# Kernel tuning notes

Hardware: AMD Instinct MI355X
Metric: run time of the kernel (lower is better)

Reference implementation:

```python
import jax, jax.numpy as jnp
import numpy as np

K = 20
NEG = jnp.float32(-1e30)

def _l2norm(x):
    # F.normalize(x, dim=1, p=2) with eps clamp
    n = jnp.sqrt(jnp.sum(x * x, axis=1, keepdims=True))
    return x / jnp.maximum(n, 1e-12)

def setup_inputs() -> dict:
    key = jax.random.key(0)
    k1, k2, k3 = jax.random.split(key, 3)
    h, w, C = 96, 96, 256
    query_label = jax.random.randint(k1, (h, w, 3), 0, 2, dtype=jnp.int64)
    color = jnp.zeros((3,), dtype=jnp.int64)
    q_feat = jax.random.normal(k2, (1, C, h, w), dtype=jnp.float32)
    s_feat = jax.random.normal(k3, (1, C, h, w), dtype=jnp.float32)
    return {"query_label": query_label, "color": color, "q_feat": q_feat, "s_feat": s_feat}

def reference(query_label, color, q_feat, s_feat):
    C = q_feat.shape[1]
    out_hw = s_feat.shape[2:]
    # mask at feature resolution (query_label already sized [h,w,3])
    mask = jnp.all(query_label == color, axis=-1).reshape(-1)      # [M]
    q = q_feat[0].transpose(1, 2, 0).reshape(-1, C)                # [M,C]
    s = s_feat[0].transpose(1, 2, 0).reshape(-1, C)                # [N,C]
    qn = _l2norm(q)
    sn = _l2norm(s)
    sim = sn @ qn.T                                                # [N,M] cosine sims
    # top-K over fg columns == top-K over full row with non-fg masked to -inf
    fg_top = jax.lax.top_k(jnp.where(mask[None, :], sim, NEG), K)[0]
    bg_top = jax.lax.top_k(jnp.where(mask[None, :], NEG, sim), K)[0]
    fg_score = jnp.mean(fg_top, axis=1).reshape(out_hw)
    bg_score = jnp.mean(bg_top, axis=1).reshape(out_hw)
    return fg_score, bg_score
```

## Files before the change

### kernel.cpp

```cpp
#include <hip/hip_runtime.h>
#include <math.h>

#define MTOT 9216
#define CDIM 256
#define KSEL 20
#define NCHUNK 4
#define CHUNKQ 2304
#define BS 32
#define QSTEP 128
#define NSTEP 18
#define NSLAB 72

typedef __attribute__((ext_vector_type(8))) short short8;
typedef __attribute__((ext_vector_type(8))) unsigned short ushort8;
typedef __attribute__((ext_vector_type(4))) float f32x4;
typedef __attribute__((ext_vector_type(2))) _Float16 h2;

__device__ __forceinline__ unsigned short f2bf(float v) {
    unsigned u = __float_as_uint(v);
    u += 0x7FFF + ((u >> 16) & 1);
    return (unsigned short)(u >> 16);
}
__device__ __forceinline__ h2 pkh2(float lo, float hi) {
    auto r = __builtin_amdgcn_cvt_pkrtz(lo, hi);
    h2 h; __builtin_memcpy(&h, &r, 4); return h;
}
__device__ __forceinline__ h2 asH2(unsigned int u) {
    h2 h; __builtin_memcpy(&h, &u, 4); return h;
}
__device__ __forceinline__ unsigned int h2u(h2 h) {
    unsigned int u; __builtin_memcpy(&u, &h, 4); return u;
}
__device__ __forceinline__ h2 h2max(h2 a, h2 b) { return __builtin_elementwise_max(a, b); }
__device__ __forceinline__ h2 h2min(h2 a, h2 b) { return __builtin_elementwise_min(a, b); }
__device__ __forceinline__ unsigned short hbits(_Float16 x) {
    unsigned short u; __builtin_memcpy(&u, &x, 2); return u;
}
__device__ __forceinline__ float hs2f(unsigned short u) {
    _Float16 x; __builtin_memcpy(&x, &u, 2); return (float)x;
}

__device__ __forceinline__ void ins20p(h2 (&l)[KSEL], h2 v) {
    v = h2max(v, l[0]);
#pragma unroll
    for (int i = 0; i < KSEL - 1; ++i) {
        h2 nxt = l[i + 1];
        l[i] = h2min(nxt, v);
        v = h2max(nxt, v);
    }
    l[KSEL - 1] = v;
}
__device__ __forceinline__ void ins20(float (&l)[KSEL], float v) {
#pragma unroll
    for (int i = 0; i < KSEL - 1; ++i) {
        float nxt = l[i + 1];
        l[i] = fminf(nxt, v);
        v = fmaxf(nxt, v);
    }
    l[KSEL - 1] = v;
}

__global__ __launch_bounds__(256) void prepconv_kernel(
    const int* __restrict__ ql, const int* __restrict__ color,
    const float* __restrict__ qf, const float* __restrict__ sf,
    int* __restrict__ cnt,
    unsigned short* __restrict__ qbt, unsigned short* __restrict__ sbt)
{
    __shared__ float tilef[32 * 257];
    __shared__ float red[256];
    __shared__ float invv[32];
    __shared__ int slotl[32];
    const int bid = blockIdx.x;
    const bool isQ = bid < (MTOT / 32);
    const int m0 = (isQ ? bid : bid - MTOT / 32) * 32;
    const float* src = isQ ? qf : sf;
    const int t = threadIdx.x;
    const int ml = t & 31, cb = t >> 5;
    float sq = 0.f;
#pragma unroll
    for (int i = 0; i < 32; ++i) {
        int c = cb * 32 + i;
        float v = src[c * MTOT + m0 + ml];
        tilef[ml * 257 + c] = v;
        sq += v * v;
    }
    red[cb * 32 + ml] = sq;
    __syncthreads();
    if (t < 32) {
        float s = 0.f;
#pragma unroll
        for (int j = 0; j < 8; ++j) s += red[j * 32 + t];
        invv[t] = 1.0f / fmaxf(sqrtf(s), 1e-12f);
        if (isQ) {
            int m = m0 + t;
            bool fg = (ql[3*m] == color[0]) & (ql[3*m+1] == color[1]) & (ql[3*m+2] == color[2]);
            slotl[t] = fg ? atomicAdd(&cnt[0], 1) : (MTOT - 1 - atomicAdd(&cnt[1], 1));
        }
    }
    __syncthreads();
    const int row = t >> 3, seg = t & 7;
    const float iv = invv[row];
    const int drow = isQ ? slotl[row] : (m0 + row);
    unsigned short* dst = (isQ ? qbt : sbt) + (size_t)drow * 256 + seg * 32;
    const float* srcr = &tilef[row * 257 + seg * 32];
#pragma unroll
    for (int ch = 0; ch < 4; ++ch) {
        ushort8 o;
#pragma unroll
        for (int e = 0; e < 8; ++e) o[e] = f2bf(srcr[ch * 8 + e] * iv);
        *(ushort8*)(dst + ch * 8) = o;
    }
}

__global__ __launch_bounds__(256, 3) void matchsim_kernel(
    const unsigned short* __restrict__ qbt, const unsigned short* __restrict__ sbt,
    const int* __restrict__ cnt, unsigned short* __restrict__ part)
{
    __shared__ __align__(16) char smem[49152];
    unsigned int* mbuf = (unsigned int*)smem;

    const int t = threadIdx.x;
    const int w = t >> 6, l = t & 63;
    const int sblk = blockIdx.x >> 2;
    const int chunk = blockIdx.x & 3;
    const int s0 = sblk * BS;
    const int q0c = chunk * CHUNKQ;
    const int fgc = cnt[0];

    {
        int row = t >> 3, cb = t & 7;
        const ushort8* gs = (const ushort8*)(sbt + (size_t)(s0 + row) * 256);
#pragma unroll
        for (int i = 0; i < 4; ++i) {
            int ch = cb + i * 8;
            ushort8 v = gs[ch];
            int byte = (row * 512 + ch * 16) ^ ((row & 7) << 4);
            *(ushort8*)(smem + byte) = v;
        }
    }

    const h2 NEG2 = { (_Float16)-65504.f, (_Float16)-65504.f };
    h2 fgl[KSEL], bgl[KSEL];
#pragma unroll
    for (int i = 0; i < KSEL; ++i) { fgl[i] = NEG2; bgl[i] = NEG2; }

    ushort8 qr[4];
    const int qrow_w = t >> 1, qhalf = t & 1;
    auto loadQ = [&](int gslab) {
        int step = gslab >> 2, slab = gslab & 3;
        const unsigned short* base =
            qbt + (size_t)(q0c + step * QSTEP + qrow_w) * 256 + slab * 64 + qhalf * 32;
#pragma unroll
        for (int i = 0; i < 4; ++i)
            qr[i] = *(const ushort8*)(base + i * 8);
    };
    loadQ(0);
    const int qwswz = (qrow_w & 7) << 4;

    const int lg = l >> 4;
    const int aq0 = w * 32 + (l & 15);
    const int aq1 = aq0 + 16;
    const int aswz0 = (aq0 & 7) << 4, aswz1 = (aq1 & 7) << 4;
    const int srow0 = l & 15, srow1 = srow0 + 16;
    const int bswz0 = (srow0 & 7) << 4, bswz1 = (srow1 & 7) << 4;

    f32x4 acc00 = {0,0,0,0}, acc01 = {0,0,0,0}, acc10 = {0,0,0,0}, acc11 = {0,0,0,0};
    int cur = 0;

    for (int gslab = 0; gslab < NSLAB; ++gslab) {
        char* Qs = smem + 16384 + cur * 16384;
#pragma unroll
        for (int i = 0; i < 4; ++i) {
            int byte = (qrow_w * 128 + qhalf * 64 + i * 16) ^ qwswz;
            *(ushort8*)(Qs + byte) = qr[i];
        }
        if (gslab + 1 < NSLAB) loadQ(gslab + 1);
        __syncthreads();
        const int slab = gslab & 3;
#pragma unroll
        for (int ks = 0; ks < 2; ++ks) {
            int ak = ks * 64 + lg * 16;
            short8 a0 = *(const short8*)(Qs + ((aq0 * 128 + ak) ^ aswz0));
            short8 a1 = *(const short8*)(Qs + ((aq1 * 128 + ak) ^ aswz1));
            int bk = slab * 128 + ks * 64 + lg * 16;
            short8 b0 = *(const short8*)(smem + ((srow0 * 512 + bk) ^ bswz0));
            short8 b1 = *(const short8*)(smem + ((srow1 * 512 + bk) ^ bswz1));
            acc00 = __builtin_amdgcn_mfma_f32_16x16x32_bf16(a0, b0, acc00, 0, 0, 0);
            acc01 = __builtin_amdgcn_mfma_f32_16x16x32_bf16(a0, b1, acc01, 0, 0, 0);
            acc10 = __builtin_amdgcn_mfma_f32_16x16x32_bf16(a1, b0, acc10, 0, 0, 0);
            acc11 = __builtin_amdgcn_mfma_f32_16x16x32_bf16(a1, b1, acc11, 0, 0, 0);
        }
        cur ^= 1;
        if (slab == 3) {
            const int step = gslab >> 2;
            const int qw0 = q0c + step * QSTEP + w * 32;
#pragma unroll
            for (int qt = 0; qt < 2; ++qt) {
                const f32x4& aS0 = qt ? acc10 : acc00;
                const f32x4& aS1 = qt ? acc11 : acc01;
                int qfirst = qw0 + qt * 16;
                if (qfirst + 16 <= fgc) {
#pragma unroll
                    for (int r = 0; r < 4; ++r) ins20p(fgl, pkh2(aS0[r], aS1[r]));
                } else if (qfirst >= fgc) {
#pragma unroll
                    for (int r = 0; r < 4; ++r) ins20p(bgl, pkh2(aS0[r], aS1[r]));
                } else {
#pragma unroll
                    for (int r = 0; r < 4; ++r) {
                        h2 v = pkh2(aS0[r], aS1[r]);
                        bool m = (qfirst + lg * 4 + r) < fgc;
                        ins20p(fgl, m ? v : NEG2);
                        ins20p(bgl, m ? NEG2 : v);
                    }
                }
            }
            acc00 = (f32x4){0,0,0,0}; acc01 = (f32x4){0,0,0,0};
            acc10 = (f32x4){0,0,0,0}; acc11 = (f32x4){0,0,0,0};
        }
    }

    __syncthreads();
    const int sp = l & 15, owner = w * 4 + lg;
    auto midx = [](int cls, int own, int spi) { return ((cls * 16 + own) * 16 + spi) * 21; };
    {
        unsigned int* df = &mbuf[midx(0, owner, sp)];
        unsigned int* db = &mbuf[midx(1, owner, sp)];
#pragma unroll
        for (int k = 0; k < KSEL; ++k) { df[k] = h2u(fgl[k]); db[k] = h2u(bgl[k]); }
    }
    __syncthreads();
    auto mergeL = [&](unsigned int* A, const unsigned int* B) {
        h2 la[KSEL];
#pragma unroll
        for (int k = 0; k < KSEL; ++k) la[k] = asH2(A[k]);
        for (int j = KSEL - 1; j >= 0; --j) {
            h2 v = asH2(B[j]);
            if (!(v.x > la[0].x || v.y > la[0].y)) break;
            ins20p(la, v);
        }
#pragma unroll
        for (int k = 0; k < KSEL; ++k) A[k] = h2u(la[k]);
    };
    {
        int cls = t >> 7, u = t & 127, spi = u & 15, j = u >> 4;
        mergeL(&mbuf[midx(cls, j, spi)], &mbuf[midx(cls, j + 8, spi)]);
    }
    __syncthreads();
    if (t < 128) {
        int cls = t >> 6, u = t & 63, spi = u & 15, j = u >> 4;
        mergeL(&mbuf[midx(cls, j, spi)], &mbuf[midx(cls, j + 4, spi)]);
    }
    __syncthreads();
    if (t < 64) {
        int cls = t >> 5, u = t & 31, spi = u & 15, j = u >> 4;
        mergeL(&mbuf[midx(cls, j, spi)], &mbuf[midx(cls, j + 2, spi)]);
    }
    __syncthreads();
    if (t < 32) {
        int cls = t >> 4, spi = t & 15;
        unsigned int* A = &mbuf[midx(cls, 0, spi)];
        const unsigned int* B = &mbuf[midx(cls, 1, spi)];
        h2 la[KSEL];
#pragma unroll
        for (int k = 0; k < KSEL; ++k) la[k] = asH2(A[k]);
        for (int j = KSEL - 1; j >= 0; --j) {
            h2 v = asH2(B[j]);
            if (!(v.x > la[0].x || v.y > la[0].y)) break;
            ins20p(la, v);
        }
        unsigned short* d0 = &part[((size_t)(s0 + spi)      * NCHUNK + chunk) * (2*KSEL) + cls*KSEL];
        unsigned short* d1 = &part[((size_t)(s0 + 16 + spi) * NCHUNK + chunk) * (2*KSEL) + cls*KSEL];
#pragma unroll
        for (int k = 0; k < KSEL; ++k) {
            d0[k] = hbits(la[k].x);
            d1[k] = hbits(la[k].y);
        }
    }
}

__global__ __launch_bounds__(256) void finalize_kernel(
    const unsigned short* __restrict__ part, float* __restrict__ out)
{
    int n = blockIdx.x * 256 + threadIdx.x;
    if (n >= MTOT) return;
    const unsigned short* base = part + (size_t)n * NCHUNK * 2 * KSEL;
#pragma unroll
    for (int cls = 0; cls < 2; ++cls) {
        float la[KSEL];
        const unsigned short* c0p = base + cls * KSEL;
#pragma unroll
        for (int k = 0; k < KSEL; ++k) la[k] = hs2f(c0p[k]);
        for (int ch = 1; ch < NCHUNK; ++ch) {
            const unsigned short* sp = base + ch * 2 * KSEL + cls * KSEL;
            for (int j = KSEL - 1; j >= 0; --j) {
                float v = hs2f(sp[j]);
                if (v <= la[0]) break;
                ins20(la, v);
            }
        }
        float s = 0.f;
#pragma unroll
        for (int k = 0; k < KSEL; ++k) s += la[k];
        out[cls * MTOT + n] = s * (1.0f / KSEL);
    }
}

extern "C" void kernel_launch(void* const* d_in, const int* in_sizes, int n_in,
                              void* d_out, int out_size, void* d_ws, size_t ws_size,
                              hipStream_t stream) {
    const int*   ql    = (const int*)d_in[0];
    const int*   color = (const int*)d_in[1];
    const float* qf    = (const float*)d_in[2];
    const float* sf    = (const float*)d_in[3];
    float* out = (float*)d_out;

    int* cnt = (int*)d_ws;
    unsigned short* qbt = (unsigned short*)(cnt + 4);
    unsigned short* sbt = qbt + (size_t)MTOT * CDIM;
    unsigned short* part = sbt + (size_t)MTOT * CDIM;

    (void)hipMemsetAsync(cnt, 0, 16, stream);
    prepconv_kernel<<<2 * (MTOT / 32), 256, 0, stream>>>(ql, color, qf, sf, cnt, qbt, sbt);
    matchsim_kernel<<<(MTOT / BS) * NCHUNK, 256, 0, stream>>>(qbt, sbt, cnt, part);
    finalize_kernel<<<MTOT / 256, 256, 0, stream>>>(part, out);
}
```

Measured before the change: 212.6 us.

## Load Q MFMA operands straight from global into registers, dropping LDS staging

The main loop no longer stages Q slabs through double-buffered shared memory with a barrier per slab. Each lane now loads its MFMA A-operand fragments directly from global memory, software-pipelined one slab ahead, and only the S tile stays in LDS. This removes 72 barriers and the LDS write/read traffic for Q. Shared memory shrinks and the launch-bounds occupancy hint rises from 3 to 4 blocks per CU, with the merge buffer stride shrunk from 21 to 20 to fit. In exchange, global loads are less coalesced (16-byte fragments spread over rows) and rely on L2/cache reuse across waves, and the stride-20 layout may cause LDS bank conflicts in the merge.

```diff
diff --git a/kernel.cpp b/kernel.cpp
--- a/kernel.cpp
+++ b/kernel.cpp
@@ -9,7 +9,6 @@
 #define BS 32
 #define QSTEP 128
 #define NSTEP 18
-#define NSLAB 72
 
 typedef __attribute__((ext_vector_type(8))) short short8;
 typedef __attribute__((ext_vector_type(8))) unsigned short ushort8;
@@ -112,11 +111,11 @@
     }
 }
 
-__global__ __launch_bounds__(256, 3) void matchsim_kernel(
+__global__ __launch_bounds__(256, 4) void matchsim_kernel(
     const unsigned short* __restrict__ qbt, const unsigned short* __restrict__ sbt,
     const int* __restrict__ cnt, unsigned short* __restrict__ part)
 {
-    __shared__ __align__(16) char smem[49152];
+    __shared__ __align__(16) char smem[40960];
     unsigned int* mbuf = (unsigned int*)smem;
 
     const int t = threadIdx.x;
@@ -138,91 +137,85 @@
             *(ushort8*)(smem + byte) = v;
         }
     }
+    __syncthreads();
 
     const h2 NEG2 = { (_Float16)-65504.f, (_Float16)-65504.f };
     h2 fgl[KSEL], bgl[KSEL];
 #pragma unroll
     for (int i = 0; i < KSEL; ++i) { fgl[i] = NEG2; bgl[i] = NEG2; }
 
-    ushort8 qr[4];
-    const int qrow_w = t >> 1, qhalf = t & 1;
-    auto loadQ = [&](int gslab) {
-        int step = gslab >> 2, slab = gslab & 3;
-        const unsigned short* base =
-            qbt + (size_t)(q0c + step * QSTEP + qrow_w) * 256 + slab * 64 + qhalf * 32;
-#pragma unroll
-        for (int i = 0; i < 4; ++i)
-            qr[i] = *(const ushort8*)(base + i * 8);
-    };
-    loadQ(0);
-    const int qwswz = (qrow_w & 7) << 4;
-
     const int lg = l >> 4;
-    const int aq0 = w * 32 + (l & 15);
-    const int aq1 = aq0 + 16;
-    const int aswz0 = (aq0 & 7) << 4, aswz1 = (aq1 & 7) << 4;
     const int srow0 = l & 15, srow1 = srow0 + 16;
     const int bswz0 = (srow0 & 7) << 4, bswz1 = (srow1 & 7) << 4;
 
+    const char* qp0 = (const char*)qbt + (size_t)(q0c + w * 32 + (l & 15)) * 512 + lg * 16;
+    const char* qp1 = qp0 + 16 * 512;
+
     f32x4 acc00 = {0,0,0,0}, acc01 = {0,0,0,0}, acc10 = {0,0,0,0}, acc11 = {0,0,0,0};
-    int cur = 0;
-
-    for (int gslab = 0; gslab < NSLAB; ++gslab) {
-        char* Qs = smem + 16384 + cur * 16384;
-#pragma unroll
-        for (int i = 0; i < 4; ++i) {
-            int byte = (qrow_w * 128 + qhalf * 64 + i * 16) ^ qwswz;
-            *(ushort8*)(Qs + byte) = qr[i];
-        }
-        if (gslab + 1 < NSLAB) loadQ(gslab + 1);
-        __syncthreads();
-        const int slab = gslab & 3;
+
+    short8 A0[4], A1[4];
+    auto prefetch = [&](int slab, short8 (&P)[4]) {
+        P[0] = *(const short8*)(qp0 + slab * 128);
+        P[1] = *(const short8*)(qp1 + slab * 128);
+        P[2] = *(const short8*)(qp0 + slab * 128 + 64);
+        P[3] = *(const short8*)(qp1 + slab * 128 + 64);
+    };
+    auto compute = [&](int slab, const short8 (&A)[4]) {
 #pragma unroll
         for (int ks = 0; ks < 2; ++ks) {
-            int ak = ks * 64 + lg * 16;
-            short8 a0 = *(const short8*)(Qs + ((aq0 * 128 + ak) ^ aswz0));
-            short8 a1 = *(const short8*)(Qs + ((aq1 * 128 + ak) ^ aswz1));
             int bk = slab * 128 + ks * 64 + lg * 16;
             short8 b0 = *(const short8*)(smem + ((srow0 * 512 + bk) ^ bswz0));
             short8 b1 = *(const short8*)(smem + ((srow1 * 512 + bk) ^ bswz1));
-            acc00 = __builtin_amdgcn_mfma_f32_16x16x32_bf16(a0, b0, acc00, 0, 0, 0);
-            acc01 = __builtin_amdgcn_mfma_f32_16x16x32_bf16(a0, b1, acc01, 0, 0, 0);
-            acc10 = __builtin_amdgcn_mfma_f32_16x16x32_bf16(a1, b0, acc10, 0, 0, 0);
-            acc11 = __builtin_amdgcn_mfma_f32_16x16x32_bf16(a1, b1, acc11, 0, 0, 0);
-        }
-        cur ^= 1;
-        if (slab == 3) {
-            const int step = gslab >> 2;
-            const int qw0 = q0c + step * QSTEP + w * 32;
-#pragma unroll
-            for (int qt = 0; qt < 2; ++qt) {
-                const f32x4& aS0 = qt ? acc10 : acc00;
-                const f32x4& aS1 = qt ? acc11 : acc01;
-                int qfirst = qw0 + qt * 16;
-                if (qfirst + 16 <= fgc) {
-#pragma unroll
-                    for (int r = 0; r < 4; ++r) ins20p(fgl, pkh2(aS0[r], aS1[r]));
-                } else if (qfirst >= fgc) {
-#pragma unroll
-                    for (int r = 0; r < 4; ++r) ins20p(bgl, pkh2(aS0[r], aS1[r]));
-                } else {
-#pragma unroll
-                    for (int r = 0; r < 4; ++r) {
-                        h2 v = pkh2(aS0[r], aS1[r]);
-                        bool m = (qfirst + lg * 4 + r) < fgc;
-                        ins20p(fgl, m ? v : NEG2);
-                        ins20p(bgl, m ? NEG2 : v);
-                    }
+            acc00 = __builtin_amdgcn_mfma_f32_16x16x32_bf16(A[ks*2+0], b0, acc00, 0, 0, 0);
+            acc01 = __builtin_amdgcn_mfma_f32_16x16x32_bf16(A[ks*2+0], b1, acc01, 0, 0, 0);
+            acc10 = __builtin_amdgcn_mfma_f32_16x16x32_bf16(A[ks*2+1], b0, acc10, 0, 0, 0);
+            acc11 = __builtin_amdgcn_mfma_f32_16x16x32_bf16(A[ks*2+1], b1, acc11, 0, 0, 0);
+        }
+    };
+
+    prefetch(0, A0);
+    for (int step = 0; step < NSTEP; ++step) {
+        prefetch(1, A1);
+        compute(0, A0);
+        prefetch(2, A0);
+        compute(1, A1);
+        prefetch(3, A1);
+        compute(2, A0);
+        if (step + 1 < NSTEP) {
+            qp0 += QSTEP * 512; qp1 += QSTEP * 512;
+            prefetch(0, A0);
+        }
+        compute(3, A1);
+
+        const int qw0 = q0c + step * QSTEP + w * 32;
+#pragma unroll
+        for (int qt = 0; qt < 2; ++qt) {
+            const f32x4& aS0 = qt ? acc10 : acc00;
+            const f32x4& aS1 = qt ? acc11 : acc01;
+            int qfirst = qw0 + qt * 16;
+            if (qfirst + 16 <= fgc) {
+#pragma unroll
+                for (int r = 0; r < 4; ++r) ins20p(fgl, pkh2(aS0[r], aS1[r]));
+            } else if (qfirst >= fgc) {
+#pragma unroll
+                for (int r = 0; r < 4; ++r) ins20p(bgl, pkh2(aS0[r], aS1[r]));
+            } else {
+#pragma unroll
+                for (int r = 0; r < 4; ++r) {
+                    h2 v = pkh2(aS0[r], aS1[r]);
+                    bool m = (qfirst + lg * 4 + r) < fgc;
+                    ins20p(fgl, m ? v : NEG2);
+                    ins20p(bgl, m ? NEG2 : v);
                 }
             }
-            acc00 = (f32x4){0,0,0,0}; acc01 = (f32x4){0,0,0,0};
-            acc10 = (f32x4){0,0,0,0}; acc11 = (f32x4){0,0,0,0};
-        }
+        }
+        acc00 = (f32x4){0,0,0,0}; acc01 = (f32x4){0,0,0,0};
+        acc10 = (f32x4){0,0,0,0}; acc11 = (f32x4){0,0,0,0};
     }
 
     __syncthreads();
     const int sp = l & 15, owner = w * 4 + lg;
-    auto midx = [](int cls, int own, int spi) { return ((cls * 16 + own) * 16 + spi) * 21; };
+    auto midx = [](int cls, int own, int spi) { return ((cls * 16 + own) * 16 + spi) * 20; };
     {
         unsigned int* df = &mbuf[midx(0, owner, sp)];
         unsigned int* db = &mbuf[midx(1, owner, sp)];
```

After: 377.1 us. 1.77x slower.
